# Performance work log

Measured on AMD Instinct MI355X. Metric: run time of the kernel, lower is better.

## Reference

```python
import jax, jax.numpy as jnp
import numpy as np

BN_EPS = 1e-5

def batchnorm2d(x, gamma, beta):
    # x: [B, H, *, *]; normalize over (B, dim2, dim3) per channel H (training-mode batch stats)
    mean = jnp.mean(x, axis=(0, 2, 3), keepdims=True)
    var = jnp.var(x, axis=(0, 2, 3), keepdims=True)
    xhat = (x - mean) * jax.lax.rsqrt(var + BN_EPS)
    return xhat * gamma[None, :, None, None] + beta[None, :, None, None]

def setup_inputs() -> dict:
    key = jax.random.key(0)
    ks = jax.random.split(key, 8)
    B, N, C = 64, 196, 768
    H = 12
    hd = C // H  # 64
    patch = 196  # img_size**2, must equal N
    x = jax.random.normal(ks[0], (B, N, C), dtype=jnp.float32)
    W_qv = jax.random.normal(ks[1], (C, 2 * C), dtype=jnp.float32) * (1.0 / np.sqrt(C))
    k_ext = jax.random.normal(ks[2], (patch, hd), dtype=jnp.float32)  # torch init: ones; randomized for testing
    attn_bias = jax.random.normal(ks[3], (1, patch), dtype=jnp.float32) * 0.02
    bn_gamma = jnp.ones((H,), dtype=jnp.float32) + 0.1 * jax.random.normal(ks[4], (H,), dtype=jnp.float32)
    bn_beta = 0.1 * jax.random.normal(ks[5], (H,), dtype=jnp.float32)
    W_proj = jax.random.normal(ks[6], (C, C), dtype=jnp.float32) * (1.0 / np.sqrt(C))
    b_proj = jnp.zeros((C,), dtype=jnp.float32)
    return {"x": x, "W_qv": W_qv, "k_ext": k_ext, "attn_bias": attn_bias,
            "bn_gamma": bn_gamma, "bn_beta": bn_beta, "W_proj": W_proj, "b_proj": b_proj}

def reference(x, W_qv, k_ext, attn_bias, bn_gamma, bn_beta, W_proj, b_proj):
    B, N, C = x.shape
    H = bn_gamma.shape[0]
    hd = C // H
    scale = hd ** -0.5
    # qv projection: [B,N,2C] -> q,v each [B,H,N,hd]
    qv = (x @ W_qv).reshape(B, N, 2, H, hd).transpose(2, 0, 3, 1, 4)
    q, v = qv[0], qv[1]
    # scores against fixed k_ext: [B,H,N,patch]
    attn = jnp.einsum('bhnd,pd->bhnp', q, k_ext)
    attn = (batchnorm2d(attn, bn_gamma, bn_beta) + attn_bias) * scale
    attn = jax.nn.softmax(attn, axis=-1)
    v = batchnorm2d(v, bn_gamma, bn_beta)
    out = jnp.einsum('bhnp,bhpd->bhnd', attn, v)  # patch == N
    out = out.transpose(0, 2, 1, 3).reshape(B, N, C)
    return out @ W_proj + b_proj
```

## Files before the change

### kernel.cpp

```cpp
#include <hip/hip_runtime.h>
#include <hip/hip_bf16.h>

typedef __bf16 b16;
typedef __bf16 b16x8 __attribute__((ext_vector_type(8)));
typedef float  f32x4 __attribute__((ext_vector_type(4)));

#define B_   64
#define N_   196
#define C_   768
#define H_   12
#define HD_  64
#define TOK  (B_*N_)
#define SCALE 0.125f

__device__ __forceinline__ void gl_lds16(const void* g, void* l){
  __builtin_amdgcn_global_load_lds((const __attribute__((address_space(1))) void*)g,
                                   (__attribute__((address_space(3))) void*)l, 16, 0, 0);
}

__global__ __launch_bounds__(256) void k_transpose_cvt(const float* __restrict__ in,
                                                       b16* __restrict__ out, int R, int C){
  __shared__ b16 tile[32][33];
  int tx = threadIdx.x, ty = threadIdx.y;
  int bx = blockIdx.x, by = blockIdx.y;
  int c = bx*32 + tx;
  #pragma unroll
  for (int i = 0; i < 32; i += 8){
    int r = by*32 + ty + i;
    tile[ty+i][tx] = (b16)in[(long)r*C + c];
  }
  __syncthreads();
  int rr = by*32 + tx;
  #pragma unroll
  for (int i = 0; i < 32; i += 8){
    int cc = bx*32 + ty + i;
    out[(long)cc*R + rr] = tile[tx][ty+i];
  }
}

__global__ __launch_bounds__(256) void k_cvt(const float* __restrict__ in, b16* __restrict__ out){
  long i = ((long)blockIdx.x*256 + threadIdx.x)*8;
  const float4* s = (const float4*)(in + i);
  float4 f0 = s[0], f1 = s[1];
  b16x8 v; v[0]=(b16)f0.x; v[1]=(b16)f0.y; v[2]=(b16)f0.z; v[3]=(b16)f0.w;
           v[4]=(b16)f1.x; v[5]=(b16)f1.y; v[6]=(b16)f1.z; v[7]=(b16)f1.w;
  *(b16x8*)(out + i) = v;
}

__global__ __launch_bounds__(256) void k_kprep(const float* __restrict__ k_ext,
                                               float* __restrict__ Kmat, float* __restrict__ ksum){
  __shared__ float ks[N_][HD_];
  int tid = threadIdx.x, blk = blockIdx.x;
  for (int i = tid; i < N_*HD_; i += 256) ks[i/HD_][i%HD_] = k_ext[i];
  __syncthreads();
  int i = tid >> 2;
  int j0 = blk*16 + (tid & 3)*4;
  float a0=0.f, a1=0.f, a2=0.f, a3=0.f;
  for (int p = 0; p < N_; ++p){
    float ki = ks[p][i];
    float4 kv = *(const float4*)&ks[p][j0];
    a0 += ki*kv.x; a1 += ki*kv.y; a2 += ki*kv.z; a3 += ki*kv.w;
  }
  Kmat[i*64+j0+0]=a0; Kmat[i*64+j0+1]=a1; Kmat[i*64+j0+2]=a2; Kmat[i*64+j0+3]=a3;
  if (blk == 0 && tid < 64){
    float s = 0.f;
    for (int p = 0; p < N_; ++p) s += ks[p][tid];
    ksum[tid] = s;
  }
}

template<int MODE>
__global__ __launch_bounds__(256) void k_gemm(const b16* __restrict__ A,
                                              const b16* __restrict__ BT,
                                              b16* __restrict__ qout, b16* __restrict__ vout,
                                              float* __restrict__ fout, const float* __restrict__ bias,
                                              const float* __restrict__ ksum, float* __restrict__ stats){
  const int NT  = (MODE == 0) ? 12 : 6;
  const int NWG = 98*NT;
  int orig = blockIdx.x;
  int q8 = NWG >> 3, r8 = NWG & 7;
  int xcd = orig & 7, loc = orig >> 3;
  int bid = (xcd < r8 ? xcd*(q8+1) : r8*(q8+1) + (xcd-r8)*q8) + loc;
  int rt = bid / NT, ct = bid % NT;
  int brow = rt*128, bcol = ct*128;

  __shared__ b16 sm[2][2][128*32];
  __shared__ float ksh[64];
  int tid = threadIdx.x, lane = tid & 63, w = tid >> 6;
  int wr = w >> 1, wc = w & 1;
  if constexpr (MODE == 0){ if (tid < 64) ksh[tid] = ksum[tid]; }

  int rsub = w*16 + (lane>>2);
  int gsrc = (lane & 3) ^ ((lane >> 3) & 3);
  const b16* gA = A  + (long)(brow + rsub)*768 + gsrc*8;
  const b16* gB = BT + (long)(bcol + rsub)*768 + gsrc*8;
  b16* lA0 = &sm[0][0][w*16*32];
  b16* lB0 = &sm[0][1][w*16*32];
  b16* lA1 = &sm[1][0][w*16*32];
  b16* lB1 = &sm[1][1][w*16*32];

#define STAGE(la, lb, kt) do{ \
    gl_lds16(gA + (kt)*32,            (la));        \
    gl_lds16(gA + (kt)*32 + 64*768,   (la) + 64*32);\
    gl_lds16(gB + (kt)*32,            (lb));        \
    gl_lds16(gB + (kt)*32 + 64*768,   (lb) + 64*32);\
  } while(0)

  f32x4 acc[4][4];
  #pragma unroll
  for (int m = 0; m < 4; ++m)
    #pragma unroll
    for (int n = 0; n < 4; ++n) acc[m][n] = (f32x4){0.f,0.f,0.f,0.f};

  STAGE(lA0, lB0, 0);
  __syncthreads();

  #pragma unroll 2
  for (int kt = 0; kt < 24; ++kt){
    int cur = kt & 1;
    if (kt < 23){
      if (cur) STAGE(lA0, lB0, kt+1);
      else     STAGE(lA1, lB1, kt+1);
    }
    const char* smA = (const char*)sm[cur][0];
    const char* smB = (const char*)sm[cur][1];
    b16x8 af[4], bf[4];
    #pragma unroll
    for (int m = 0; m < 4; ++m){
      int row = wr*64 + m*16 + (lane & 15);
      af[m] = *(const b16x8*)(smA + row*64 + (((lane>>4) ^ ((row>>1)&3))<<4));
    }
    #pragma unroll
    for (int n = 0; n < 4; ++n){
      int row = wc*64 + n*16 + (lane & 15);
      bf[n] = *(const b16x8*)(smB + row*64 + (((lane>>4) ^ ((row>>1)&3))<<4));
    }
    #pragma unroll
    for (int m = 0; m < 4; ++m)
      #pragma unroll
      for (int n = 0; n < 4; ++n)
        acc[m][n] = __builtin_amdgcn_mfma_f32_16x16x32_bf16(af[m], bf[n], acc[m][n], 0, 0, 0);
    __syncthreads();
  }
#undef STAGE

  if constexpr (MODE == 0){
    #pragma unroll
    for (int m = 0; m < 4; ++m){
      #pragma unroll
      for (int n = 0; n < 4; ++n){
        int col = bcol + wc*64 + n*16 + (lane & 15);
        int two = (col >= 768) ? 1 : 0;
        int hc = col - two*768;
        int hh = hc >> 6, d = hc & 63;
        b16* dst = two ? vout : qout;
        #pragma unroll
        for (int j = 0; j < 4; ++j){
          int r2 = brow + wr*64 + m*16 + ((lane>>4)<<2) + j;
          int bq = r2 / 196;
          int nn = r2 - bq*196;
          dst[((bq*12 + hh)*196 + nn)*64 + d] = (b16)acc[m][n][j];
        }
      }
    }
    {
      bool isV = (bcol >= 768);
      float a_acc = 0.f, b_acc = 0.f;
      #pragma unroll
      for (int n = 0; n < 4; ++n){
        int d = n*16 + (lane & 15);
        float s = 0.f, s2 = 0.f;
        #pragma unroll
        for (int m = 0; m < 4; ++m)
          #pragma unroll
          for (int j = 0; j < 4; ++j){
            float v = acc[m][n][j];
            s += v; s2 += v*v;
          }
        if (isV){ a_acc += s; b_acc += s2; }
        else      a_acc += s * ksh[d];
      }
      #pragma unroll
      for (int off = 1; off < 64; off <<= 1){
        a_acc += __shfl_xor(a_acc, off, 64);
        b_acc += __shfl_xor(b_acc, off, 64);
      }
      if (lane == 0){
        if (isV){
          int hv = 2*(ct - 6) + wc;
          atomicAdd(&stats[24 + hv], a_acc);
          atomicAdd(&stats[36 + hv], b_acc);
        } else {
          int hq = 2*ct + wc;
          atomicAdd(&stats[hq], a_acc);
        }
      }
    }
  } else {
    #pragma unroll
    for (int m = 0; m < 4; ++m){
      #pragma unroll
      for (int n = 0; n < 4; ++n){
        int col = bcol + wc*64 + n*16 + (lane & 15);
        float bv = bias[col];
        #pragma unroll
        for (int j = 0; j < 4; ++j){
          int r2 = brow + wr*64 + m*16 + ((lane>>4)<<2) + j;
          fout[(long)r2*768 + col] = acc[m][n][j] + bv;
        }
      }
    }
  }
}

__global__ __launch_bounds__(256) void k_gram(const b16* __restrict__ qb, float* __restrict__ G){
  __shared__ b16 qT[64*232];
  int tid = threadIdx.x, lane = tid & 63, w = tid >> 6;
  int h = blockIdx.x % 12, bg = blockIdx.x / 12;
  f32x4 acc[4];
  #pragma unroll
  for (int n = 0; n < 4; ++n) acc[n] = (f32x4){0.f,0.f,0.f,0.f};
  #pragma unroll 1
  for (int r = 0; r < 2; ++r){
    int b = bg*2 + r;
    const b16* src = qb + ((long)(b*12 + h))*196*64;
    int d = lane;
    for (int p0 = w*8; p0 < 224; p0 += 32){
      b16x8 w8;
      #pragma unroll
      for (int j = 0; j < 8; ++j){
        int p = p0 + j;
        w8[j] = (p < 196) ? src[p*64 + d] : (b16)0.f;
      }
      *(b16x8*)(qT + d*232 + p0) = w8;
    }
    __syncthreads();
    #pragma unroll
    for (int ks = 0; ks < 7; ++ks){
      int t0 = ks*32;
      b16x8 af = *(const b16x8*)(qT + (16*w + (lane&15))*232 + t0 + ((lane>>4)<<3));
      #pragma unroll
      for (int n = 0; n < 4; ++n){
        b16x8 bf = *(const b16x8*)(qT + (16*n + (lane&15))*232 + t0 + ((lane>>4)<<3));
        acc[n] = __builtin_amdgcn_mfma_f32_16x16x32_bf16(af, bf, acc[n], 0, 0, 0);
      }
    }
    __syncthreads();
  }
  float* Gh = G + h*4096;
  #pragma unroll
  for (int n = 0; n < 4; ++n)
    #pragma unroll
    for (int j = 0; j < 4; ++j){
      int i  = 16*w + ((lane>>4)<<2) + j;
      int jj = 16*n + (lane&15);
      atomicAdd(&Gh[i*64 + jj], acc[n][j]);
    }
}

__global__ __launch_bounds__(256) void k_sfin(const float* __restrict__ G, const float* __restrict__ Kmat,
                                              const float* __restrict__ stats, const float* __restrict__ gamma,
                                              const float* __restrict__ beta, float* __restrict__ coef){
  int h = blockIdx.x, tid = threadIdx.x;
  const float* Gh = G + h*4096;
  float s = 0.f;
  #pragma unroll
  for (int k = 0; k < 16; ++k) s += Gh[tid + k*256]*Kmat[tid + k*256];
  #pragma unroll
  for (int off = 1; off < 64; off <<= 1) s += __shfl_xor(s, off, 64);
  __shared__ float red[4];
  if ((tid & 63) == 0) red[tid>>6] = s;
  __syncthreads();
  if (tid == 0){
    float S2 = red[0]+red[1]+red[2]+red[3];
    const float cntS = 2458624.f, cntV = 802816.f;
    float S1 = stats[h], VS = stats[24+h], VS2 = stats[36+h];
    float ms = S1/cntS;
    float vars = S2/cntS - ms*ms;
    float alpha = gamma[h]*SCALE*rsqrtf(vars + 1e-5f);
    float mv = VS/cntV;
    float varv = VS2/cntV - mv*mv;
    float a = gamma[h]*rsqrtf(varv + 1e-5f);
    coef[h*4+0] = alpha;
    coef[h*4+1] = a;
    coef[h*4+2] = beta[h] - a*mv;
  }
}

__global__ __launch_bounds__(256, 2) void k_attn(const b16* __restrict__ qb, const b16* __restrict__ vb,
                                                 const float* __restrict__ k_ext,
                                                 const float* __restrict__ attn_bias,
                                                 const float* __restrict__ coef,
                                                 b16* __restrict__ Ob){
  __shared__ b16 ksh[196*64];
  __shared__ b16 vsh[64*216];
  __shared__ b16 psh[4][16*200];
  __shared__ float bsh[196];

  int tid = threadIdx.x, lane = tid & 63, wid = tid >> 6;
  int bh = blockIdx.x;
  int h = bh % 12, b = bh / 12;
  const b16* qt = qb + (long)bh*N_*64;
  const b16* vt = vb + (long)bh*N_*64;
  float alpha = coef[h*4+0], av = coef[h*4+1], cv = coef[h*4+2];

  for (int c = tid; c < 196*8; c += 256){
    int p = c >> 3, g = c & 7;
    const float4* src = (const float4*)(k_ext + p*64 + g*8);
    float4 f0 = src[0], f1 = src[1];
    b16x8 v; v[0]=(b16)f0.x; v[1]=(b16)f0.y; v[2]=(b16)f0.z; v[3]=(b16)f0.w;
             v[4]=(b16)f1.x; v[5]=(b16)f1.y; v[6]=(b16)f1.z; v[7]=(b16)f1.w;
    *(b16x8*)((char*)ksh + p*128 + ((g ^ (p&7))<<4)) = v;
  }
  for (int p = tid; p < 196; p += 256) bsh[p] = attn_bias[p]*SCALE;
  {
    int d = tid & 63;
    for (int p0 = (tid>>6)*8; p0 < 196; p0 += 32){
      b16x8 w;
      #pragma unroll
      for (int j = 0; j < 8; ++j){
        int p = p0 + j;
        w[j] = (p < 196) ? vt[p*64 + d] : (b16)0.f;
      }
      *(b16x8*)((char*)vsh + d*432 + p0*2) = w;
    }
  }
  __syncthreads();

  for (int rt = wid; rt < 13; rt += 4){
    int n0 = rt*16;
    int qrow = n0 + (lane & 15); if (qrow > 195) qrow = 195;
    b16x8 a0 = *(const b16x8*)((const char*)qt + qrow*128 +      ((lane>>4)<<4));
    b16x8 a1 = *(const b16x8*)((const char*)qt + qrow*128 + 64 + ((lane>>4)<<4));

    f32x4 sc[13];
    #pragma unroll
    for (int ct = 0; ct < 13; ++ct){
      int p = ct*16 + (lane & 15); int pc = p > 195 ? 195 : p;
      b16x8 b0 = *(const b16x8*)((const char*)ksh + pc*128 + ((( (lane>>4))   ^ (pc&7))<<4));
      b16x8 b1 = *(const b16x8*)((const char*)ksh + pc*128 + (((4+(lane>>4))  ^ (pc&7))<<4));
      f32x4 z = {0.f,0.f,0.f,0.f};
      z = __builtin_amdgcn_mfma_f32_16x16x32_bf16(a0, b0, z, 0, 0, 0);
      z = __builtin_amdgcn_mfma_f32_16x16x32_bf16(a1, b1, z, 0, 0, 0);
      sc[ct] = z;
    }
    int pcol = lane & 15;
    float mx[4] = {-1e30f,-1e30f,-1e30f,-1e30f};
    #pragma unroll
    for (int ct = 0; ct < 13; ++ct){
      int p = ct*16 + pcol;
      bool valid = (p < 196);
      float badd = valid ? bsh[p < 196 ? p : 0] : 0.f;
      #pragma unroll
      for (int j = 0; j < 4; ++j){
        float lv = valid ? (sc[ct][j]*alpha + badd) : -1e30f;
        sc[ct][j] = lv;
        mx[j] = fmaxf(mx[j], lv);
      }
    }
    #pragma unroll
    for (int off = 1; off < 16; off <<= 1)
      #pragma unroll
      for (int j = 0; j < 4; ++j) mx[j] = fmaxf(mx[j], __shfl_xor(mx[j], off, 64));
    float sm[4] = {0.f,0.f,0.f,0.f};
    #pragma unroll
    for (int ct = 0; ct < 13; ++ct)
      #pragma unroll
      for (int j = 0; j < 4; ++j){
        float e = __expf(sc[ct][j] - mx[j]);
        sc[ct][j] = e; sm[j] += e;
      }
    #pragma unroll
    for (int off = 1; off < 16; off <<= 1)
      #pragma unroll
      for (int j = 0; j < 4; ++j) sm[j] += __shfl_xor(sm[j], off, 64);
    float rs[4];
    #pragma unroll
    for (int j = 0; j < 4; ++j) rs[j] = 1.f/sm[j];

    b16* pw = psh[wid];
    #pragma unroll
    for (int ct = 0; ct < 12; ++ct){
      int p = ct*16 + pcol;
      #pragma unroll
      for (int j = 0; j < 4; ++j){
        int r = ((lane>>4)<<2) + j;
        pw[r*200 + p] = (b16)(sc[ct][j]*rs[j]);
      }
    }
    float pt12[4];
    #pragma unroll
    for (int j = 0; j < 4; ++j) pt12[j] = sc[12][j]*rs[j];

    __asm__ volatile("s_waitcnt lgkmcnt(0)" ::: "memory");
    __builtin_amdgcn_sched_barrier(0);

    f32x4 o[4];
    #pragma unroll
    for (int dt = 0; dt < 4; ++dt) o[dt] = (f32x4){0.f,0.f,0.f,0.f};
    #pragma unroll
    for (int pt = 0; pt < 6; ++pt){
      b16x8 pa = *(const b16x8*)((const char*)pw + (lane&15)*400 + pt*64 + ((lane>>4)<<4));
      #pragma unroll
      for (int dt = 0; dt < 4; ++dt){
        b16x8 vf = *(const b16x8*)((const char*)vsh + (dt*16 + (lane&15))*432 + pt*64 + ((lane>>4)<<4));
        o[dt] = __builtin_amdgcn_mfma_f32_16x16x32_bf16(pa, vf, o[dt], 0, 0, 0);
      }
    }
    #pragma unroll
    for (int e = 0; e < 4; ++e){
      float pe[4];
      #pragma unroll
      for (int j = 0; j < 4; ++j) pe[j] = __shfl(pt12[j], (lane & 48) + e, 64);
      #pragma unroll
      for (int dt = 0; dt < 4; ++dt){
        b16 vv = *((const b16*)((const char*)vsh + (dt*16 + (lane&15))*432 + (192+e)*2));
        float vvf = (float)vv;
        #pragma unroll
        for (int j = 0; j < 4; ++j) o[dt][j] += pe[j]*vvf;
      }
    }
    #pragma unroll
    for (int dt = 0; dt < 4; ++dt)
      #pragma unroll
      for (int j = 0; j < 4; ++j){
        int n = n0 + ((lane>>4)<<2) + j;
        if (n < 196){
          long idx = ((long)(b*196 + n))*768 + h*64 + dt*16 + (lane&15);
          Ob[idx] = (b16)(av*o[dt][j] + cv);
        }
      }
  }
}

extern "C" void kernel_launch(void* const* d_in, const int* in_sizes, int n_in,
                              void* d_out, int out_size, void* d_ws, size_t ws_size,
                              hipStream_t stream){
  const float* x         = (const float*)d_in[0];
  const float* W_qv      = (const float*)d_in[1];
  const float* k_ext     = (const float*)d_in[2];
  const float* attn_bias = (const float*)d_in[3];
  const float* bn_gamma  = (const float*)d_in[4];
  const float* bn_beta   = (const float*)d_in[5];
  const float* W_proj    = (const float*)d_in[6];
  const float* b_proj    = (const float*)d_in[7];
  float* out = (float*)d_out;

  char* ws = (char*)d_ws;
  const long SZ = 19267584;
  b16*   q_buf   = (b16*)(ws);
  b16*   v_buf   = (b16*)(ws + SZ);
  b16*   O_buf   = (b16*)(ws + 2*SZ);
  b16*   x_bf16  = (b16*)(ws + 2*SZ);
  b16*   W_qvT   = (b16*)(ws + 3*SZ);
  b16*   W_projT = (b16*)(ws + 3*SZ + 2359296);
  float* Kmat    = (float*)(ws + 3*SZ + 3538944);
  float* ksum    = Kmat + 4096;
  float* stats   = ksum + 64;
  float* coef    = stats + 48;
  float* Ggram   = coef + 48;

  hipMemsetAsync(stats, 0, 48*sizeof(float), stream);
  hipMemsetAsync(Ggram, 0, 12*4096*sizeof(float), stream);

  dim3 tb(32, 8);
  k_transpose_cvt<<<dim3(1536/32, 768/32), tb, 0, stream>>>(W_qv,   W_qvT,   768, 1536);
  k_transpose_cvt<<<dim3(768/32,  768/32), tb, 0, stream>>>(W_proj, W_projT, 768, 768);
  k_cvt<<<4704, 256, 0, stream>>>(x, x_bf16);
  k_kprep<<<4, 256, 0, stream>>>(k_ext, Kmat, ksum);
  k_gemm<0><<<98*12, 256, 0, stream>>>(x_bf16, W_qvT, q_buf, v_buf, nullptr, nullptr, ksum, stats);
  k_gram<<<384, 256, 0, stream>>>(q_buf, Ggram);
  k_sfin<<<12, 256, 0, stream>>>(Ggram, Kmat, stats, bn_gamma, bn_beta, coef);
  k_attn<<<768, 256, 0, stream>>>(q_buf, v_buf, k_ext, attn_bias, coef, O_buf);
  k_gemm<1><<<98*6, 256, 0, stream>>>(O_buf, W_projT, nullptr, nullptr, out, b_proj, nullptr, nullptr);
}
```

Baseline: 199.7 us.

## Keep the next K-tile's loads in flight across GEMM barriers with explicit vmcnt waits

Result: faster. 189.2 us (-5.3%).

```diff
diff --git a/kernel.cpp b/kernel.cpp
--- a/kernel.cpp
+++ b/kernel.cpp
@@ -85,10 +85,8 @@
   int brow = rt*128, bcol = ct*128;
 
   __shared__ b16 sm[2][2][128*32];
-  __shared__ float ksh[64];
   int tid = threadIdx.x, lane = tid & 63, w = tid >> 6;
   int wr = w >> 1, wc = w & 1;
-  if constexpr (MODE == 0){ if (tid < 64) ksh[tid] = ksum[tid]; }
 
   int rsub = w*16 + (lane>>2);
   int gsrc = (lane & 3) ^ ((lane >> 3) & 3);
@@ -106,6 +104,27 @@
     gl_lds16(gB + (kt)*32 + 64*768,   (lb) + 64*32);\
   } while(0)
 
+#define COMPUTE(cur) do{ \
+    const char* smA = (const char*)sm[cur][0]; \
+    const char* smB = (const char*)sm[cur][1]; \
+    b16x8 af[4], bf[4]; \
+    _Pragma("unroll") \
+    for (int m = 0; m < 4; ++m){ \
+      int row = wr*64 + m*16 + (lane & 15); \
+      af[m] = *(const b16x8*)(smA + row*64 + (((lane>>4) ^ ((row>>1)&3))<<4)); \
+    } \
+    _Pragma("unroll") \
+    for (int n = 0; n < 4; ++n){ \
+      int row = wc*64 + n*16 + (lane & 15); \
+      bf[n] = *(const b16x8*)(smB + row*64 + (((lane>>4) ^ ((row>>1)&3))<<4)); \
+    } \
+    _Pragma("unroll") \
+    for (int m = 0; m < 4; ++m) \
+      _Pragma("unroll") \
+      for (int n = 0; n < 4; ++n) \
+        acc[m][n] = __builtin_amdgcn_mfma_f32_16x16x32_bf16(af[m], bf[n], acc[m][n], 0, 0, 0); \
+  } while(0)
+
   f32x4 acc[4][4];
   #pragma unroll
   for (int m = 0; m < 4; ++m)
@@ -113,35 +132,28 @@
     for (int n = 0; n < 4; ++n) acc[m][n] = (f32x4){0.f,0.f,0.f,0.f};
 
   STAGE(lA0, lB0, 0);
-  __syncthreads();
-
-  #pragma unroll 2
-  for (int kt = 0; kt < 24; ++kt){
+  STAGE(lA1, lB1, 1);
+
+  #pragma unroll 1
+  for (int kt = 0; kt < 23; ++kt){
     int cur = kt & 1;
-    if (kt < 23){
-      if (cur) STAGE(lA0, lB0, kt+1);
-      else     STAGE(lA1, lB1, kt+1);
-    }
-    const char* smA = (const char*)sm[cur][0];
-    const char* smB = (const char*)sm[cur][1];
-    b16x8 af[4], bf[4];
-    #pragma unroll
-    for (int m = 0; m < 4; ++m){
-      int row = wr*64 + m*16 + (lane & 15);
-      af[m] = *(const b16x8*)(smA + row*64 + (((lane>>4) ^ ((row>>1)&3))<<4));
-    }
-    #pragma unroll
-    for (int n = 0; n < 4; ++n){
-      int row = wc*64 + n*16 + (lane & 15);
-      bf[n] = *(const b16x8*)(smB + row*64 + (((lane>>4) ^ ((row>>1)&3))<<4));
-    }
-    #pragma unroll
-    for (int m = 0; m < 4; ++m)
-      #pragma unroll
-      for (int n = 0; n < 4; ++n)
-        acc[m][n] = __builtin_amdgcn_mfma_f32_16x16x32_bf16(af[m], bf[n], acc[m][n], 0, 0, 0);
-    __syncthreads();
-  }
+    asm volatile("s_waitcnt vmcnt(4)" ::: "memory");
+    __builtin_amdgcn_s_barrier();
+    asm volatile("" ::: "memory");
+    COMPUTE(cur);
+    asm volatile("" ::: "memory");
+    __builtin_amdgcn_s_barrier();
+    asm volatile("" ::: "memory");
+    if (kt < 22){
+      if (cur == 0) STAGE(lA0, lB0, kt+2);
+      else          STAGE(lA1, lB1, kt+2);
+    }
+  }
+  asm volatile("s_waitcnt vmcnt(0)" ::: "memory");
+  __builtin_amdgcn_s_barrier();
+  asm volatile("" ::: "memory");
+  COMPUTE(1);
+#undef COMPUTE
 #undef STAGE
 
   if constexpr (MODE == 0){
@@ -178,7 +190,7 @@
             s += v; s2 += v*v;
           }
         if (isV){ a_acc += s; b_acc += s2; }
-        else      a_acc += s * ksh[d];
+        else      a_acc += s * ksum[d];
       }
       #pragma unroll
       for (int off = 1; off < 64; off <<= 1){
```

## Restructure GEMM into 256x128 tiles with triple-buffered LDS and interleaved MFMA scheduling

Applied to the files above, without the earlier changes.

Measured after the change: 190.8 us. 1.05x faster.

```diff
diff --git a/kernel.cpp b/kernel.cpp
--- a/kernel.cpp
+++ b/kernel.cpp
@@ -70,96 +70,125 @@
 }
 
 template<int MODE>
-__global__ __launch_bounds__(256) void k_gemm(const b16* __restrict__ A,
-                                              const b16* __restrict__ BT,
-                                              b16* __restrict__ qout, b16* __restrict__ vout,
-                                              float* __restrict__ fout, const float* __restrict__ bias,
-                                              const float* __restrict__ ksum, float* __restrict__ stats){
+__global__ __launch_bounds__(512, 2) void k_gemm(const b16* __restrict__ A,
+                                                 const b16* __restrict__ BT,
+                                                 b16* __restrict__ qout, b16* __restrict__ vout,
+                                                 float* __restrict__ fout, const float* __restrict__ bias,
+                                                 const float* __restrict__ ksum, float* __restrict__ stats){
   const int NT  = (MODE == 0) ? 12 : 6;
-  const int NWG = 98*NT;
+  const int NWG = 49*NT;
+  extern __shared__ char smc[];
   int orig = blockIdx.x;
   int q8 = NWG >> 3, r8 = NWG & 7;
   int xcd = orig & 7, loc = orig >> 3;
   int bid = (xcd < r8 ? xcd*(q8+1) : r8*(q8+1) + (xcd-r8)*q8) + loc;
   int rt = bid / NT, ct = bid % NT;
-  int brow = rt*128, bcol = ct*128;
-
-  __shared__ b16 sm[2][2][128*32];
-  __shared__ float ksh[64];
+  int brow = rt*256, bcol = ct*128;
+
   int tid = threadIdx.x, lane = tid & 63, w = tid >> 6;
-  int wr = w >> 1, wc = w & 1;
-  if constexpr (MODE == 0){ if (tid < 64) ksh[tid] = ksum[tid]; }
-
-  int rsub = w*16 + (lane>>2);
-  int gsrc = (lane & 3) ^ ((lane >> 3) & 3);
-  const b16* gA = A  + (long)(brow + rsub)*768 + gsrc*8;
-  const b16* gB = BT + (long)(bcol + rsub)*768 + gsrc*8;
-  b16* lA0 = &sm[0][0][w*16*32];
-  b16* lB0 = &sm[0][1][w*16*32];
-  b16* lA1 = &sm[1][0][w*16*32];
-  b16* lB1 = &sm[1][1][w*16*32];
-
-#define STAGE(la, lb, kt) do{ \
-    gl_lds16(gA + (kt)*32,            (la));        \
-    gl_lds16(gA + (kt)*32 + 64*768,   (la) + 64*32);\
-    gl_lds16(gB + (kt)*32,            (lb));        \
-    gl_lds16(gB + (kt)*32 + 64*768,   (lb) + 64*32);\
-  } while(0)
-
-  f32x4 acc[4][4];
-  #pragma unroll
-  for (int m = 0; m < 4; ++m)
-    #pragma unroll
-    for (int n = 0; n < 4; ++n) acc[m][n] = (f32x4){0.f,0.f,0.f,0.f};
-
-  STAGE(lA0, lB0, 0);
-  __syncthreads();
-
-  #pragma unroll 2
-  for (int kt = 0; kt < 24; ++kt){
-    int cur = kt & 1;
-    if (kt < 23){
-      if (cur) STAGE(lA0, lB0, kt+1);
-      else     STAGE(lA1, lB1, kt+1);
-    }
-    const char* smA = (const char*)sm[cur][0];
-    const char* smB = (const char*)sm[cur][1];
-    b16x8 af[4], bf[4];
-    #pragma unroll
-    for (int m = 0; m < 4; ++m){
-      int row = wr*64 + m*16 + (lane & 15);
-      af[m] = *(const b16x8*)(smA + row*64 + (((lane>>4) ^ ((row>>1)&3))<<4));
-    }
-    #pragma unroll
-    for (int n = 0; n < 4; ++n){
-      int row = wc*64 + n*16 + (lane & 15);
-      bf[n] = *(const b16x8*)(smB + row*64 + (((lane>>4) ^ ((row>>1)&3))<<4));
-    }
-    #pragma unroll
-    for (int m = 0; m < 4; ++m)
-      #pragma unroll
-      for (int n = 0; n < 4; ++n)
-        acc[m][n] = __builtin_amdgcn_mfma_f32_16x16x32_bf16(af[m], bf[n], acc[m][n], 0, 0, 0);
-    __syncthreads();
-  }
-#undef STAGE
+  int wr = w >> 2, wc = w & 3;
+
+  int lrow8 = lane >> 3;
+  int g8 = (lane & 7) ^ lrow8;
+  const b16* gA = A  + (long)(brow + w*8 + lrow8)*768 + g8*8;
+  const b16* gB = BT + (long)(bcol + w*8 + lrow8)*768 + g8*8;
+
+#define STAGE_A01(bb, t) do{ long ko = (long)(t)*64; \
+    gl_lds16(gA + ko,           smc + (bb) + (0*8+w)*1024); \
+    gl_lds16(gA + 64*768 + ko,  smc + (bb) + (1*8+w)*1024); } while(0)
+#define STAGE_A23(bb, t) do{ long ko = (long)(t)*64; \
+    gl_lds16(gA + 128*768 + ko, smc + (bb) + (2*8+w)*1024); \
+    gl_lds16(gA + 192*768 + ko, smc + (bb) + (3*8+w)*1024); } while(0)
+#define STAGE_B(bb, t) do{ long ko = (long)(t)*64; \
+    gl_lds16(gB + ko,           smc + (bb) + 32768 + (0*8+w)*1024); \
+    gl_lds16(gB + 64*768 + ko,  smc + (bb) + 32768 + (1*8+w)*1024); } while(0)
+
+#define LDA(bb, mm, kh) (*(const b16x8*)(smc + (bb) + (wr*128 + (mm)*16 + (lane&15))*128 \
+                          + ((((kh)*4 + (lane>>4)) ^ (lane&7))<<4)))
+#define LDB(bb, nn, kh) (*(const b16x8*)(smc + (bb) + 32768 + (wc*32 + (nn)*16 + (lane&15))*128 \
+                          + ((((kh)*4 + (lane>>4)) ^ (lane&7))<<4)))
+
+  f32x4 acc[8][2];
+  #pragma unroll
+  for (int m = 0; m < 8; ++m){ acc[m][0] = (f32x4){0.f,0.f,0.f,0.f}; acc[m][1] = (f32x4){0.f,0.f,0.f,0.f}; }
+
+  STAGE_A01(0, 0); STAGE_A23(0, 0); STAGE_B(0, 0);
+  STAGE_A01(49152, 1); STAGE_A23(49152, 1); STAGE_B(49152, 1);
+
+  #pragma unroll 1
+  for (int kt = 0; kt < 12; ++kt){
+    int bb = (kt % 3) * 49152;
+    int sb = ((kt+2) % 3) * 49152;
+    bool do_stage = (kt < 10);
+    if (kt < 11) asm volatile("s_waitcnt vmcnt(6)" ::: "memory");
+    else         asm volatile("s_waitcnt vmcnt(0)" ::: "memory");
+    __builtin_amdgcn_s_barrier();
+    asm volatile("" ::: "memory");
+
+    b16x8 af[8], bf0, bf1;
+    #pragma unroll
+    for (int m = 0; m < 8; ++m) af[m] = LDA(bb, m, 0);
+    bf0 = LDB(bb, 0, 0);
+    bf1 = LDB(bb, 1, 0);
+    if (do_stage) STAGE_A01(sb, kt+2);
+    asm volatile("s_waitcnt lgkmcnt(0)" ::: "memory");
+    __builtin_amdgcn_sched_barrier(0);
+    __builtin_amdgcn_s_setprio(1);
+    #pragma unroll
+    for (int m = 0; m < 8; ++m)
+      acc[m][0] = __builtin_amdgcn_mfma_f32_16x16x32_bf16(af[m], bf0, acc[m][0], 0, 0, 0);
+    __builtin_amdgcn_s_setprio(0);
+    __builtin_amdgcn_sched_barrier(0);
+    if (do_stage) STAGE_A23(sb, kt+2);
+    __builtin_amdgcn_sched_barrier(0);
+    __builtin_amdgcn_s_setprio(1);
+    #pragma unroll
+    for (int m = 0; m < 8; ++m)
+      acc[m][1] = __builtin_amdgcn_mfma_f32_16x16x32_bf16(af[m], bf1, acc[m][1], 0, 0, 0);
+    __builtin_amdgcn_s_setprio(0);
+    __builtin_amdgcn_sched_barrier(0);
+    #pragma unroll
+    for (int m = 0; m < 8; ++m) af[m] = LDA(bb, m, 1);
+    bf0 = LDB(bb, 0, 1);
+    bf1 = LDB(bb, 1, 1);
+    if (do_stage) STAGE_B(sb, kt+2);
+    asm volatile("s_waitcnt lgkmcnt(0)" ::: "memory");
+    __builtin_amdgcn_sched_barrier(0);
+    __builtin_amdgcn_s_setprio(1);
+    #pragma unroll
+    for (int m = 0; m < 8; ++m)
+      acc[m][0] = __builtin_amdgcn_mfma_f32_16x16x32_bf16(af[m], bf0, acc[m][0], 0, 0, 0);
+    __builtin_amdgcn_s_setprio(0);
+    __builtin_amdgcn_sched_barrier(0);
+    __builtin_amdgcn_s_setprio(1);
+    #pragma unroll
+    for (int m = 0; m < 8; ++m)
+      acc[m][1] = __builtin_amdgcn_mfma_f32_16x16x32_bf16(af[m], bf1, acc[m][1], 0, 0, 0);
+    __builtin_amdgcn_s_setprio(0);
+    __builtin_amdgcn_sched_barrier(0);
+  }
+#undef STAGE_A01
+#undef STAGE_A23
+#undef STAGE_B
+#undef LDA
+#undef LDB
 
   if constexpr (MODE == 0){
     #pragma unroll
-    for (int m = 0; m < 4; ++m){
-      #pragma unroll
-      for (int n = 0; n < 4; ++n){
-        int col = bcol + wc*64 + n*16 + (lane & 15);
+    for (int m = 0; m < 8; ++m){
+      #pragma unroll
+      for (int n = 0; n < 2; ++n){
+        int col = bcol + wc*32 + n*16 + (lane & 15);
         int two = (col >= 768) ? 1 : 0;
         int hc = col - two*768;
         int hh = hc >> 6, d = hc & 63;
         b16* dst = two ? vout : qout;
         #pragma unroll
         for (int j = 0; j < 4; ++j){
-          int r2 = brow + wr*64 + m*16 + ((lane>>4)<<2) + j;
+          int r2 = brow + wr*128 + m*16 + ((lane>>4)<<2) + j;
           int bq = r2 / 196;
-          int nn = r2 - bq*196;
-          dst[((bq*12 + hh)*196 + nn)*64 + d] = (b16)acc[m][n][j];
+          int nn2 = r2 - bq*196;
+          dst[((bq*12 + hh)*196 + nn2)*64 + d] = (b16)acc[m][n][j];
         }
       }
     }
@@ -167,18 +196,18 @@
       bool isV = (bcol >= 768);
       float a_acc = 0.f, b_acc = 0.f;
       #pragma unroll
-      for (int n = 0; n < 4; ++n){
-        int d = n*16 + (lane & 15);
+      for (int n = 0; n < 2; ++n){
+        int d = (wc & 1)*32 + n*16 + (lane & 15);
         float s = 0.f, s2 = 0.f;
         #pragma unroll
-        for (int m = 0; m < 4; ++m)
+        for (int m = 0; m < 8; ++m)
           #pragma unroll
           for (int j = 0; j < 4; ++j){
             float v = acc[m][n][j];
             s += v; s2 += v*v;
           }
         if (isV){ a_acc += s; b_acc += s2; }
-        else      a_acc += s * ksh[d];
+        else      a_acc += s * ksum[d];
       }
       #pragma unroll
       for (int off = 1; off < 64; off <<= 1){
@@ -187,25 +216,25 @@
       }
       if (lane == 0){
         if (isV){
-          int hv = 2*(ct - 6) + wc;
+          int hv = 2*(ct - 6) + (wc >> 1);
           atomicAdd(&stats[24 + hv], a_acc);
           atomicAdd(&stats[36 + hv], b_acc);
         } else {
-          int hq = 2*ct + wc;
+          int hq = 2*ct + (wc >> 1);
           atomicAdd(&stats[hq], a_acc);
         }
       }
     }
   } else {
     #pragma unroll
-    for (int m = 0; m < 4; ++m){
-      #pragma unroll
-      for (int n = 0; n < 4; ++n){
-        int col = bcol + wc*64 + n*16 + (lane & 15);
+    for (int m = 0; m < 8; ++m){
+      #pragma unroll
+      for (int n = 0; n < 2; ++n){
+        int col = bcol + wc*32 + n*16 + (lane & 15);
         float bv = bias[col];
         #pragma unroll
         for (int j = 0; j < 4; ++j){
-          int r2 = brow + wr*64 + m*16 + ((lane>>4)<<2) + j;
+          int r2 = brow + wr*128 + m*16 + ((lane>>4)<<2) + j;
           fout[(long)r2*768 + col] = acc[m][n][j] + bv;
         }
       }
@@ -468,9 +497,9 @@
   k_transpose_cvt<<<dim3(768/32,  768/32), tb, 0, stream>>>(W_proj, W_projT, 768, 768);
   k_cvt<<<4704, 256, 0, stream>>>(x, x_bf16);
   k_kprep<<<4, 256, 0, stream>>>(k_ext, Kmat, ksum);
-  k_gemm<0><<<98*12, 256, 0, stream>>>(x_bf16, W_qvT, q_buf, v_buf, nullptr, nullptr, ksum, stats);
+  k_gemm<0><<<49*12, 512, 147456, stream>>>(x_bf16, W_qvT, q_buf, v_buf, nullptr, nullptr, ksum, stats);
   k_gram<<<384, 256, 0, stream>>>(q_buf, Ggram);
   k_sfin<<<12, 256, 0, stream>>>(Ggram, Kmat, stats, bn_gamma, bn_beta, coef);
   k_attn<<<768, 256, 0, stream>>>(q_buf, v_buf, k_ext, attn_bias, coef, O_buf);
-  k_gemm<1><<<98*6, 256, 0, stream>>>(O_buf, W_projT, nullptr, nullptr, out, b_proj, nullptr, nullptr);
-}
+  k_gemm<1><<<49*6, 512, 147456, stream>>>(O_buf, W_projT, nullptr, nullptr, out, b_proj, nullptr, nullptr);
+}
```
